# Performance work log

Measured on AMD Instinct MI355X. Metric: run time of the kernel, lower is better.

The kernel has to match this reference:

```python
import jax, jax.numpy as jnp
import numpy as np

H, D = 16, 64          # num_heads, head_dim
OUT = H * D            # out_dim = 1024
W1, W2 = 32, 32        # sliding windows
EPS_NORM = 1e-7
EPS_LN = 1e-5


def setup_inputs() -> dict:
    key = jax.random.key(0)
    ks = jax.random.split(key, 6)
    B, S, IN = 2, 2048, 1024
    x = jax.random.normal(ks[0], (B, S, IN), dtype=jnp.float32)
    scale = 0.02
    W_Q = jax.random.normal(ks[1], (IN, OUT), dtype=jnp.float32) * scale
    W_K = jax.random.normal(ks[2], (IN, OUT), dtype=jnp.float32) * scale
    W_V = jax.random.normal(ks[3], (IN, OUT), dtype=jnp.float32) * scale
    W_Kp = jax.random.normal(ks[4], (IN, OUT), dtype=jnp.float32) * scale
    W_O = jax.random.normal(ks[5], (OUT, OUT), dtype=jnp.float32) * scale
    ln_gamma = jnp.ones((OUT,), dtype=jnp.float32)
    ln_beta = jnp.zeros((OUT,), dtype=jnp.float32)
    return {"x": x, "W_Q": W_Q, "W_K": W_K, "W_V": W_V, "W_Kp": W_Kp,
            "W_O": W_O, "ln_gamma": ln_gamma, "ln_beta": ln_beta}


def _l2norm(t):
    return t / (jnp.linalg.norm(t, axis=-1, keepdims=True) + EPS_NORM)


def reference(x, W_Q, W_K, W_V, W_Kp, W_O, ln_gamma, ln_beta):
    B, S, _ = x.shape
    # projections -> (B, S, H, D)
    Q = _l2norm((x @ W_Q).reshape(B, S, H, D))
    K = _l2norm((x @ W_K).reshape(B, S, H, D))
    Kp = _l2norm((x @ W_Kp).reshape(B, S, H, D))
    V = (x @ W_V).reshape(B, S, H, D)
    # windowed keys/values (last w1/w2 positions, as in the PyTorch fallback)
    K_win = K[:, -W1:]
    Kp_win = Kp[:, -W2:]
    V_win = V[:, -W1:]
    Vp_win = V[:, -W2:]
    # triple product A_ijk = q.k.k' / sqrt(D) -> (B, S, H, w1, w2)
    A = jnp.einsum('bshd,bjhd,bkhd->bshjk', Q, K_win, Kp_win) / jnp.sqrt(jnp.float32(D))
    # causal window mask: allow j <= i + w1 - S and k <= i + w2 - S
    s_idx = jnp.arange(S)[:, None, None]
    j_idx = jnp.arange(W1)[None, :, None]
    k_idx = jnp.arange(W2)[None, None, :]
    mask = (j_idx > s_idx + (W1 - S)) | (k_idx > s_idx + (W2 - S))  # (S, w1, w2)
    neg_inf = jnp.float32(-jnp.inf)
    A = jnp.where(mask[None, :, None, :, :], neg_inf, A)
    # joint softmax over (j, k); fully-masked query rows produce zeros
    A_flat = A.reshape(B, S, H, W1 * W2)
    all_masked = jnp.all(A_flat == neg_inf, axis=-1, keepdims=True)
    A_safe = jnp.where(all_masked, 0.0, A_flat)
    P = jax.nn.softmax(A_safe, axis=-1)
    P = jnp.where(all_masked, 0.0, P).reshape(B, S, H, W1, W2)
    # value outer-product weighting (V' = V)
    Z = jnp.einsum('bshjk,bjhd,bkhd->bshd', P, V_win, Vp_win)
    out = Z.reshape(B, S, OUT) @ W_O
    out = out + x  # residual (shapes match)
    # LayerNorm
    mu = jnp.mean(out, axis=-1, keepdims=True)
    var = jnp.mean((out - mu) ** 2, axis=-1, keepdims=True)
    out = (out - mu) / jnp.sqrt(var + EPS_LN) * ln_gamma + ln_beta
    return out
```

## Files before the change

kernel.cpp:

```cpp
#include <hip/hip_runtime.h>
#include <math.h>


#define XS 68

#define YP_STR   262144
#define NKS_P    8
#define ZF_OFF   (NKS_P * YP_STR)
#define DP_OFF   (ZF_OFF + 65536)
#define DP_STR   65536
#define NKS_W    16

__global__ __launch_bounds__(256, 4) void proj_kernel(
    const float* __restrict__ x,
    const float* __restrict__ Wq, const float* __restrict__ Wk,
    const float* __restrict__ Wkp, const float* __restrict__ Wv,
    float* __restrict__ Y) {
  __shared__ float xs[64 * 65];
  __shared__ float wl[64 * 68];
  const int tid  = threadIdx.x;
  const int cb   = blockIdx.x;
  const int ks   = blockIdx.y;
  const int col0 = cb * 64;
  const int z    = cb >> 4;
  const int colz = col0 & 1023;
  const float* __restrict__ W =
      (z == 0) ? Wq : ((z == 1) ? Wk : ((z == 2) ? Wkp : Wv));

  const int wave = __builtin_amdgcn_readfirstlane(tid >> 6);
  const int lane = tid & 63;

  float acc[16];
  #pragma unroll
  for (int c = 0; c < 16; c++) acc[c] = 0.f;

  for (int cc = 0; cc < 2; cc++) {
    const int kb = ks * 128 + cc * 64;
    #pragma unroll
    for (int i = 0; i < 4; i++) {
      int e = i * 256 + tid;
      int r = e >> 4, q = e & 15;
      int b = r >> 5, t = r & 31;
      float4 v = *(const float4*)(x + ((b * 2048 + 2016 + t) * 1024 + kb + q * 4));
      xs[(q * 4 + 0) * 65 + r] = v.x;
      xs[(q * 4 + 1) * 65 + r] = v.y;
      xs[(q * 4 + 2) * 65 + r] = v.z;
      xs[(q * 4 + 3) * 65 + r] = v.w;
    }
    #pragma unroll
    for (int i = 0; i < 4; i++) {
      int e = i * 256 + tid;
      int r = e >> 4, q = e & 15;
      float4 v = *(const float4*)(W + (size_t)(kb + r) * 1024 + colz + q * 4);
      float* d = wl + r * 68 + q * 4;
      d[0] = v.x; d[1] = v.y; d[2] = v.z; d[3] = v.w;
    }
    __syncthreads();

    const float* __restrict__ wbase = wl + wave * 16;
    #pragma unroll 4
    for (int kk = 0; kk < 64; kk++) {
      float xv = xs[kk * 65 + lane];
      const float* __restrict__ wrow = wbase + kk * 68;
      #pragma unroll
      for (int c = 0; c < 16; c++) acc[c] = fmaf(xv, wrow[c], acc[c]);
    }
    __syncthreads();
  }

  #pragma unroll
  for (int c = 0; c < 16; c++) xs[lane * 65 + wave * 16 + c] = acc[c];
  __syncthreads();
  float* __restrict__ Yo = Y + ks * YP_STR + col0;
  #pragma unroll
  for (int i = 0; i < 16; i++) {
    int r = wave * 16 + i;
    Yo[r * 4096 + lane] = xs[r * 65 + lane];
  }
}

__global__ __launch_bounds__(256) void attn_kernel(
    const float* __restrict__ Y, float* __restrict__ Zout) {
  __shared__ float Kn[32 * XS], Kp[32 * XS], Vs[32 * XS];
  __shared__ float Pt[4][32 * 33];
  __shared__ float qs[4][64];
  const int tid = threadIdx.x;
  const int wave = tid >> 6, lane = tid & 63;
  const int h = blockIdx.y, b = blockIdx.z;

  #pragma unroll
  for (int i = 0; i < 8; i++) {
    int e = i * 256 + tid;
    int row = e >> 6, d = e & 63;
    int src = (b * 32 + row) * 4096 + h * 64 + d;
    float kn = 0.f, kp = 0.f, vv = 0.f;
    #pragma unroll
    for (int p = 0; p < NKS_P; p++) {
      const float* Yp = Y + p * YP_STR + src;
      kn += Yp[1024]; kp += Yp[2048]; vv += Yp[3072];
    }
    Kn[row * XS + d] = kn; Kp[row * XS + d] = kp; Vs[row * XS + d] = vv;
  }
  __syncthreads();

  for (int rr = 0; rr < 8; rr++) {
    int row = wave * 8 + rr;
    float kv = Kn[row * XS + lane];
    float s2 = kv * kv;
    #pragma unroll
    for (int off = 1; off < 64; off <<= 1) s2 += __shfl_xor(s2, off);
    Kn[row * XS + lane] = kv * (1.f / (sqrtf(s2) + 1e-7f));
    float pv = Kp[row * XS + lane];
    float p2 = pv * pv;
    #pragma unroll
    for (int off = 1; off < 64; off <<= 1) p2 += __shfl_xor(p2, off);
    Kp[row * XS + lane] = pv * (1.f / (sqrtf(p2) + 1e-7f));
  }
  __syncthreads();

  const int m = blockIdx.x * 4 + wave;
  const int r = b * 32 + m;

  float q = 0.f;
  #pragma unroll
  for (int p = 0; p < NKS_P; p++) q += Y[p * YP_STR + r * 4096 + h * 64 + lane];
  float q2 = q * q;
  #pragma unroll
  for (int off = 1; off < 64; off <<= 1) q2 += __shfl_xor(q2, off);
  q *= (1.f / (sqrtf(q2) + 1e-7f));
  qs[wave][lane] = q;
  __builtin_amdgcn_wave_barrier();

  const int lj = lane >> 3, lk = lane & 7;
  float acc[4][4];
  #pragma unroll
  for (int a = 0; a < 4; a++)
    #pragma unroll
    for (int c = 0; c < 4; c++) acc[a][c] = 0.f;

  const float* qw = qs[wave];
  for (int dq = 0; dq < 16; dq++) {
    float4 q4 = *(const float4*)(qw + dq * 4);
    float4 t4[4], kp4[4];
    #pragma unroll
    for (int tj = 0; tj < 4; tj++) {
      float4 kv = *(const float4*)(Kn + (lj * 4 + tj) * XS + dq * 4);
      t4[tj].x = q4.x * kv.x; t4[tj].y = q4.y * kv.y;
      t4[tj].z = q4.z * kv.z; t4[tj].w = q4.w * kv.w;
    }
    #pragma unroll
    for (int tk = 0; tk < 4; tk++)
      kp4[tk] = *(const float4*)(Kp + (lk * 4 + tk) * XS + dq * 4);
    #pragma unroll
    for (int tj = 0; tj < 4; tj++)
      #pragma unroll
      for (int tk = 0; tk < 4; tk++)
        acc[tj][tk] += t4[tj].x * kp4[tk].x + t4[tj].y * kp4[tk].y
                     + t4[tj].z * kp4[tk].z + t4[tj].w * kp4[tk].w;
  }

  float amax = -1e30f;
  #pragma unroll
  for (int tj = 0; tj < 4; tj++)
    #pragma unroll
    for (int tk = 0; tk < 4; tk++) {
      int j = lj * 4 + tj, k = lk * 4 + tk;
      if (j <= m && k <= m) amax = fmaxf(amax, acc[tj][tk] * 0.125f);
    }
  #pragma unroll
  for (int off = 1; off < 64; off <<= 1) amax = fmaxf(amax, __shfl_xor(amax, off));

  float lsum = 0.f;
  float* ptw = Pt[wave];
  #pragma unroll
  for (int tj = 0; tj < 4; tj++)
    #pragma unroll
    for (int tk = 0; tk < 4; tk++) {
      int j = lj * 4 + tj, k = lk * 4 + tk;
      float e = 0.f;
      if (j <= m && k <= m) e = __expf(acc[tj][tk] * 0.125f - amax);
      lsum += e;
      ptw[k * 33 + j] = e;
    }
  #pragma unroll
  for (int off = 1; off < 64; off <<= 1) lsum += __shfl_xor(lsum, off);
  float inv = 1.f / lsum;
  __builtin_amdgcn_wave_barrier();

  float vreg[32];
  #pragma unroll
  for (int k = 0; k < 32; k++) vreg[k] = Vs[k * XS + lane];
  float zacc = 0.f;
  for (int k = 0; k <= m; k++) {
    float g = 0.f;
    #pragma unroll
    for (int j = 0; j < 32; j++) g += ptw[k * 33 + j] * vreg[j];
    zacc += g * vreg[k];
  }
  Zout[r * 1024 + h * 64 + lane] = zacc * inv;
}

__global__ __launch_bounds__(256, 4) void wo_kernel(
    const float* __restrict__ Zr, const float* __restrict__ Wo,
    float* __restrict__ Dp) {
  __shared__ float xs[64 * 65];
  __shared__ float wl[64 * 68];
  const int tid  = threadIdx.x;
  const int col0 = blockIdx.x * 64;
  const int ks   = blockIdx.y;
  const int kb   = ks * 64;

  const int wave = __builtin_amdgcn_readfirstlane(tid >> 6);
  const int lane = tid & 63;

  #pragma unroll
  for (int i = 0; i < 4; i++) {
    int e = i * 256 + tid;
    int r = e >> 4, q = e & 15;
    float4 v = *(const float4*)(Zr + r * 1024 + kb + q * 4);
    xs[(q * 4 + 0) * 65 + r] = v.x;
    xs[(q * 4 + 1) * 65 + r] = v.y;
    xs[(q * 4 + 2) * 65 + r] = v.z;
    xs[(q * 4 + 3) * 65 + r] = v.w;
  }
  #pragma unroll
  for (int i = 0; i < 4; i++) {
    int e = i * 256 + tid;
    int r = e >> 4, q = e & 15;
    float4 v = *(const float4*)(Wo + (size_t)(kb + r) * 1024 + col0 + q * 4);
    float* d = wl + r * 68 + q * 4;
    d[0] = v.x; d[1] = v.y; d[2] = v.z; d[3] = v.w;
  }
  __syncthreads();

  float acc[16];
  #pragma unroll
  for (int c = 0; c < 16; c++) acc[c] = 0.f;

  const float* __restrict__ wbase = wl + wave * 16;
  #pragma unroll 4
  for (int kk = 0; kk < 64; kk++) {
    float xv = xs[kk * 65 + lane];
    const float* __restrict__ wrow = wbase + kk * 68;
    #pragma unroll
    for (int c = 0; c < 16; c++) acc[c] = fmaf(xv, wrow[c], acc[c]);
  }

  __syncthreads();
  #pragma unroll
  for (int c = 0; c < 16; c++) xs[lane * 65 + wave * 16 + c] = acc[c];
  __syncthreads();
  float* __restrict__ D = Dp + ks * DP_STR + col0;
  #pragma unroll
  for (int i = 0; i < 16; i++) {
    int r = wave * 16 + i;
    D[r * 1024 + lane] = xs[r * 65 + lane];
  }
}

__global__ __launch_bounds__(256, 4) void ln_kernel(
    const float4* __restrict__ x4, const float4* __restrict__ dp4,
    const float4* __restrict__ g4, const float4* __restrict__ b4,
    float4* __restrict__ out4) {
  const int tid = threadIdx.x;
  const int wave = tid >> 6, lane = tid & 63;
  const int row = blockIdx.x * 4 + wave;
  const int b = row >> 11, s = row & 2047;

  float4 v[4];
  #pragma unroll
  for (int i = 0; i < 4; i++) v[i] = x4[row * 256 + i * 64 + lane];
  if (s >= 2016) {
    int drow = b * 32 + (s - 2016);
    #pragma unroll
    for (int p = 0; p < NKS_W; p++) {
      #pragma unroll
      for (int i = 0; i < 4; i++) {
        float4 d = dp4[p * 16384 + drow * 256 + i * 64 + lane];
        v[i].x += d.x; v[i].y += d.y; v[i].z += d.z; v[i].w += d.w;
      }
    }
  }
  float sum = 0.f, ss = 0.f;
  #pragma unroll
  for (int i = 0; i < 4; i++) {
    sum += v[i].x + v[i].y + v[i].z + v[i].w;
    ss  += v[i].x * v[i].x + v[i].y * v[i].y + v[i].z * v[i].z + v[i].w * v[i].w;
  }
  #pragma unroll
  for (int off = 1; off < 64; off <<= 1) {
    sum += __shfl_xor(sum, off);
    ss  += __shfl_xor(ss, off);
  }
  float mu   = sum * (1.f / 1024.f);
  float var  = ss * (1.f / 1024.f) - mu * mu;
  float rstd = rsqrtf(var + 1e-5f);

  #pragma unroll
  for (int i = 0; i < 4; i++) {
    float4 g = g4[i * 64 + lane];
    float4 be = b4[i * 64 + lane];
    float4 o;
    o.x = (v[i].x - mu) * rstd * g.x + be.x;
    o.y = (v[i].y - mu) * rstd * g.y + be.y;
    o.z = (v[i].z - mu) * rstd * g.z + be.z;
    o.w = (v[i].w - mu) * rstd * g.w + be.w;
    out4[row * 256 + i * 64 + lane] = o;
  }
}

extern "C" void kernel_launch(void* const* d_in, const int* in_sizes, int n_in,
                              void* d_out, int out_size, void* d_ws, size_t ws_size,
                              hipStream_t stream) {
  const float* x   = (const float*)d_in[0];
  const float* Wq  = (const float*)d_in[1];
  const float* Wk  = (const float*)d_in[2];
  const float* Wv  = (const float*)d_in[3];
  const float* Wkp = (const float*)d_in[4];
  const float* Wo  = (const float*)d_in[5];
  const float* gam = (const float*)d_in[6];
  const float* bet = (const float*)d_in[7];
  float* out = (float*)d_out;
  float* ws  = (float*)d_ws;

  hipLaunchKernelGGL(proj_kernel, dim3(64, NKS_P), dim3(256), 0, stream,
                     x, Wq, Wk, Wkp, Wv, ws);
  hipLaunchKernelGGL(attn_kernel, dim3(8, 16, 2), dim3(256), 0, stream,
                     ws, ws + ZF_OFF);
  hipLaunchKernelGGL(wo_kernel, dim3(16, NKS_W), dim3(256), 0, stream,
                     ws + ZF_OFF, Wo, ws + DP_OFF);
  hipLaunchKernelGGL(ln_kernel, dim3(1024), dim3(256), 0, stream,
                     (const float4*)x, (const float4*)(ws + DP_OFF),
                     (const float4*)gam, (const float4*)bet, (float4*)out);
}
```

Before: 136.4 us.

## Fuse non-window LayerNorm into projection launch and use 4x4 register tiles

Query rows outside the last 32 positions get zero attention output, so their LayerNorm needs only x. That work now runs in extra blocks of the projection launch, overlapping the projection GEMM, and the final LN kernel handles only the 64 window rows. The projection and W_O GEMM tiles switch from one-column-per-lane with 16 accumulators to 4x4 register micro-tiles with float4 shared-memory loads and direct float4 stores, removing the shared-memory transpose epilogue. The cost is a mixed-role kernel whose LN blocks may compete with the GEMM blocks for CU slots.

```diff
diff --git a/kernel.cpp b/kernel.cpp
--- a/kernel.cpp
+++ b/kernel.cpp
@@ -3,6 +3,7 @@
 
 
 #define XS 68
+#define WS 68
 
 #define YP_STR   262144
 #define NKS_P    8
@@ -11,71 +12,124 @@
 #define DP_STR   65536
 #define NKS_W    16
 
-__global__ __launch_bounds__(256, 4) void proj_kernel(
+__device__ __forceinline__ void ln_row(
+    const float4* __restrict__ x4, const float4* __restrict__ g4,
+    const float4* __restrict__ b4, float4* __restrict__ out4,
+    int row, int lane) {
+  float4 v[4];
+  #pragma unroll
+  for (int i = 0; i < 4; i++) v[i] = x4[row * 256 + i * 64 + lane];
+  float sum = 0.f, ss = 0.f;
+  #pragma unroll
+  for (int i = 0; i < 4; i++) {
+    sum += v[i].x + v[i].y + v[i].z + v[i].w;
+    ss  += v[i].x * v[i].x + v[i].y * v[i].y + v[i].z * v[i].z + v[i].w * v[i].w;
+  }
+  #pragma unroll
+  for (int off = 1; off < 64; off <<= 1) {
+    sum += __shfl_xor(sum, off);
+    ss  += __shfl_xor(ss, off);
+  }
+  float mu   = sum * (1.f / 1024.f);
+  float rstd = rsqrtf(ss * (1.f / 1024.f) - mu * mu + 1e-5f);
+  #pragma unroll
+  for (int i = 0; i < 4; i++) {
+    float4 g  = g4[i * 64 + lane];
+    float4 be = b4[i * 64 + lane];
+    float4 o;
+    o.x = (v[i].x - mu) * rstd * g.x + be.x;
+    o.y = (v[i].y - mu) * rstd * g.y + be.y;
+    o.z = (v[i].z - mu) * rstd * g.z + be.z;
+    o.w = (v[i].w - mu) * rstd * g.w + be.w;
+    out4[row * 256 + i * 64 + lane] = o;
+  }
+}
+
+__global__ __launch_bounds__(256, 4) void proj_ln_kernel(
     const float* __restrict__ x,
     const float* __restrict__ Wq, const float* __restrict__ Wk,
     const float* __restrict__ Wkp, const float* __restrict__ Wv,
-    float* __restrict__ Y) {
-  __shared__ float xs[64 * 65];
-  __shared__ float wl[64 * 68];
-  const int tid  = threadIdx.x;
-  const int cb   = blockIdx.x;
-  const int ks   = blockIdx.y;
-  const int col0 = cb * 64;
-  const int z    = cb >> 4;
-  const int colz = col0 & 1023;
-  const float* __restrict__ W =
-      (z == 0) ? Wq : ((z == 1) ? Wk : ((z == 2) ? Wkp : Wv));
-
-  const int wave = __builtin_amdgcn_readfirstlane(tid >> 6);
-  const int lane = tid & 63;
-
-  float acc[16];
-  #pragma unroll
-  for (int c = 0; c < 16; c++) acc[c] = 0.f;
-
-  for (int cc = 0; cc < 2; cc++) {
-    const int kb = ks * 128 + cc * 64;
+    const float* __restrict__ gam, const float* __restrict__ bet,
+    float* __restrict__ Y, float* __restrict__ out) {
+  __shared__ float xs[64 * WS];
+  __shared__ float wl[64 * WS];
+  const int tid = threadIdx.x;
+  const int bid = blockIdx.x;
+
+  if (bid < 512) {
+    const int cb   = bid & 63;
+    const int ks   = bid >> 6;
+    const int col0 = cb * 64;
+    const int z    = cb >> 4;
+    const int colz = col0 & 1023;
+    const float* __restrict__ W =
+        (z == 0) ? Wq : ((z == 1) ? Wk : ((z == 2) ? Wkp : Wv));
+    const int tc = tid & 15, tr = tid >> 4;
+
+    float acc[4][4];
+    #pragma unroll
+    for (int i = 0; i < 4; i++)
+      #pragma unroll
+      for (int j = 0; j < 4; j++) acc[i][j] = 0.f;
+
+    for (int cc = 0; cc < 2; cc++) {
+      const int kb = ks * 128 + cc * 64;
+      #pragma unroll
+      for (int i = 0; i < 4; i++) {
+        int e = i * 256 + tid;
+        int r = e >> 4, q = e & 15;
+        int b = r >> 5, t = r & 31;
+        float4 v = *(const float4*)(x + ((b * 2048 + 2016 + t) * 1024 + kb + q * 4));
+        xs[(q * 4 + 0) * WS + r] = v.x;
+        xs[(q * 4 + 1) * WS + r] = v.y;
+        xs[(q * 4 + 2) * WS + r] = v.z;
+        xs[(q * 4 + 3) * WS + r] = v.w;
+        float4 w = *(const float4*)(W + (size_t)(kb + r) * 1024 + colz + q * 4);
+        *(float4*)(wl + r * WS + q * 4) = w;
+      }
+      __syncthreads();
+
+      #pragma unroll 8
+      for (int kk = 0; kk < 64; kk++) {
+        float4 xv = *(const float4*)(xs + kk * WS + tr * 4);
+        float4 wv = *(const float4*)(wl + kk * WS + tc * 4);
+        acc[0][0] = fmaf(xv.x, wv.x, acc[0][0]);
+        acc[0][1] = fmaf(xv.x, wv.y, acc[0][1]);
+        acc[0][2] = fmaf(xv.x, wv.z, acc[0][2]);
+        acc[0][3] = fmaf(xv.x, wv.w, acc[0][3]);
+        acc[1][0] = fmaf(xv.y, wv.x, acc[1][0]);
+        acc[1][1] = fmaf(xv.y, wv.y, acc[1][1]);
+        acc[1][2] = fmaf(xv.y, wv.z, acc[1][2]);
+        acc[1][3] = fmaf(xv.y, wv.w, acc[1][3]);
+        acc[2][0] = fmaf(xv.z, wv.x, acc[2][0]);
+        acc[2][1] = fmaf(xv.z, wv.y, acc[2][1]);
+        acc[2][2] = fmaf(xv.z, wv.z, acc[2][2]);
+        acc[2][3] = fmaf(xv.z, wv.w, acc[2][3]);
+        acc[3][0] = fmaf(xv.w, wv.x, acc[3][0]);
+        acc[3][1] = fmaf(xv.w, wv.y, acc[3][1]);
+        acc[3][2] = fmaf(xv.w, wv.z, acc[3][2]);
+        acc[3][3] = fmaf(xv.w, wv.w, acc[3][3]);
+      }
+      __syncthreads();
+    }
+
+    float* __restrict__ Yo = Y + ks * YP_STR + col0;
     #pragma unroll
     for (int i = 0; i < 4; i++) {
-      int e = i * 256 + tid;
-      int r = e >> 4, q = e & 15;
-      int b = r >> 5, t = r & 31;
-      float4 v = *(const float4*)(x + ((b * 2048 + 2016 + t) * 1024 + kb + q * 4));
-      xs[(q * 4 + 0) * 65 + r] = v.x;
-      xs[(q * 4 + 1) * 65 + r] = v.y;
-      xs[(q * 4 + 2) * 65 + r] = v.z;
-      xs[(q * 4 + 3) * 65 + r] = v.w;
-    }
-    #pragma unroll
-    for (int i = 0; i < 4; i++) {
-      int e = i * 256 + tid;
-      int r = e >> 4, q = e & 15;
-      float4 v = *(const float4*)(W + (size_t)(kb + r) * 1024 + colz + q * 4);
-      float* d = wl + r * 68 + q * 4;
-      d[0] = v.x; d[1] = v.y; d[2] = v.z; d[3] = v.w;
-    }
-    __syncthreads();
-
-    const float* __restrict__ wbase = wl + wave * 16;
-    #pragma unroll 4
-    for (int kk = 0; kk < 64; kk++) {
-      float xv = xs[kk * 65 + lane];
-      const float* __restrict__ wrow = wbase + kk * 68;
-      #pragma unroll
-      for (int c = 0; c < 16; c++) acc[c] = fmaf(xv, wrow[c], acc[c]);
-    }
-    __syncthreads();
-  }
-
-  #pragma unroll
-  for (int c = 0; c < 16; c++) xs[lane * 65 + wave * 16 + c] = acc[c];
-  __syncthreads();
-  float* __restrict__ Yo = Y + ks * YP_STR + col0;
-  #pragma unroll
-  for (int i = 0; i < 16; i++) {
-    int r = wave * 16 + i;
-    Yo[r * 4096 + lane] = xs[r * 65 + lane];
+      float4 o = make_float4(acc[i][0], acc[i][1], acc[i][2], acc[i][3]);
+      *(float4*)(Yo + (tr * 4 + i) * 4096 + tc * 4) = o;
+    }
+  } else {
+    const int wave = tid >> 6, lane = tid & 63;
+    const int gw = (bid - 512) * 4 + wave;
+    const float4* x4 = (const float4*)x;
+    const float4* g4 = (const float4*)gam;
+    const float4* b4 = (const float4*)bet;
+    float4* out4 = (float4*)out;
+    for (int idx = gw; idx < 4032; idx += 1792) {
+      int row = (idx < 2016) ? idx : idx + 32;
+      ln_row(x4, g4, b4, out4, row, lane);
+    }
   }
 }
 
@@ -203,82 +257,82 @@
 __global__ __launch_bounds__(256, 4) void wo_kernel(
     const float* __restrict__ Zr, const float* __restrict__ Wo,
     float* __restrict__ Dp) {
-  __shared__ float xs[64 * 65];
-  __shared__ float wl[64 * 68];
+  __shared__ float zs[64 * WS];
+  __shared__ float wl[64 * WS];
   const int tid  = threadIdx.x;
   const int col0 = blockIdx.x * 64;
   const int ks   = blockIdx.y;
   const int kb   = ks * 64;
-
-  const int wave = __builtin_amdgcn_readfirstlane(tid >> 6);
-  const int lane = tid & 63;
+  const int tc = tid & 15, tr = tid >> 4;
 
   #pragma unroll
   for (int i = 0; i < 4; i++) {
     int e = i * 256 + tid;
     int r = e >> 4, q = e & 15;
     float4 v = *(const float4*)(Zr + r * 1024 + kb + q * 4);
-    xs[(q * 4 + 0) * 65 + r] = v.x;
-    xs[(q * 4 + 1) * 65 + r] = v.y;
-    xs[(q * 4 + 2) * 65 + r] = v.z;
-    xs[(q * 4 + 3) * 65 + r] = v.w;
-  }
-  #pragma unroll
-  for (int i = 0; i < 4; i++) {
-    int e = i * 256 + tid;
-    int r = e >> 4, q = e & 15;
-    float4 v = *(const float4*)(Wo + (size_t)(kb + r) * 1024 + col0 + q * 4);
-    float* d = wl + r * 68 + q * 4;
-    d[0] = v.x; d[1] = v.y; d[2] = v.z; d[3] = v.w;
+    zs[(q * 4 + 0) * WS + r] = v.x;
+    zs[(q * 4 + 1) * WS + r] = v.y;
+    zs[(q * 4 + 2) * WS + r] = v.z;
+    zs[(q * 4 + 3) * WS + r] = v.w;
+    float4 w = *(const float4*)(Wo + (size_t)(kb + r) * 1024 + col0 + q * 4);
+    *(float4*)(wl + r * WS + q * 4) = w;
   }
   __syncthreads();
 
-  float acc[16];
-  #pragma unroll
-  for (int c = 0; c < 16; c++) acc[c] = 0.f;
-
-  const float* __restrict__ wbase = wl + wave * 16;
-  #pragma unroll 4
+  float acc[4][4];
+  #pragma unroll
+  for (int i = 0; i < 4; i++)
+    #pragma unroll
+    for (int j = 0; j < 4; j++) acc[i][j] = 0.f;
+
+  #pragma unroll 8
   for (int kk = 0; kk < 64; kk++) {
-    float xv = xs[kk * 65 + lane];
-    const float* __restrict__ wrow = wbase + kk * 68;
-    #pragma unroll
-    for (int c = 0; c < 16; c++) acc[c] = fmaf(xv, wrow[c], acc[c]);
-  }
-
-  __syncthreads();
-  #pragma unroll
-  for (int c = 0; c < 16; c++) xs[lane * 65 + wave * 16 + c] = acc[c];
-  __syncthreads();
+    float4 xv = *(const float4*)(zs + kk * WS + tr * 4);
+    float4 wv = *(const float4*)(wl + kk * WS + tc * 4);
+    acc[0][0] = fmaf(xv.x, wv.x, acc[0][0]);
+    acc[0][1] = fmaf(xv.x, wv.y, acc[0][1]);
+    acc[0][2] = fmaf(xv.x, wv.z, acc[0][2]);
+    acc[0][3] = fmaf(xv.x, wv.w, acc[0][3]);
+    acc[1][0] = fmaf(xv.y, wv.x, acc[1][0]);
+    acc[1][1] = fmaf(xv.y, wv.y, acc[1][1]);
+    acc[1][2] = fmaf(xv.y, wv.z, acc[1][2]);
+    acc[1][3] = fmaf(xv.y, wv.w, acc[1][3]);
+    acc[2][0] = fmaf(xv.z, wv.x, acc[2][0]);
+    acc[2][1] = fmaf(xv.z, wv.y, acc[2][1]);
+    acc[2][2] = fmaf(xv.z, wv.z, acc[2][2]);
+    acc[2][3] = fmaf(xv.z, wv.w, acc[2][3]);
+    acc[3][0] = fmaf(xv.w, wv.x, acc[3][0]);
+    acc[3][1] = fmaf(xv.w, wv.y, acc[3][1]);
+    acc[3][2] = fmaf(xv.w, wv.z, acc[3][2]);
+    acc[3][3] = fmaf(xv.w, wv.w, acc[3][3]);
+  }
+
   float* __restrict__ D = Dp + ks * DP_STR + col0;
   #pragma unroll
-  for (int i = 0; i < 16; i++) {
-    int r = wave * 16 + i;
-    D[r * 1024 + lane] = xs[r * 65 + lane];
-  }
-}
-
-__global__ __launch_bounds__(256, 4) void ln_kernel(
+  for (int i = 0; i < 4; i++) {
+    float4 o = make_float4(acc[i][0], acc[i][1], acc[i][2], acc[i][3]);
+    *(float4*)(D + (tr * 4 + i) * 1024 + tc * 4) = o;
+  }
+}
+
+__global__ __launch_bounds__(256, 4) void ln_win_kernel(
     const float4* __restrict__ x4, const float4* __restrict__ dp4,
     const float4* __restrict__ g4, const float4* __restrict__ b4,
     float4* __restrict__ out4) {
   const int tid = threadIdx.x;
   const int wave = tid >> 6, lane = tid & 63;
-  const int row = blockIdx.x * 4 + wave;
-  const int b = row >> 11, s = row & 2047;
+  const int wr  = blockIdx.x * 4 + wave;
+  const int row = (wr >> 5) * 2048 + 2016 + (wr & 31);
 
   float4 v[4];
   #pragma unroll
   for (int i = 0; i < 4; i++) v[i] = x4[row * 256 + i * 64 + lane];
-  if (s >= 2016) {
-    int drow = b * 32 + (s - 2016);
-    #pragma unroll
-    for (int p = 0; p < NKS_W; p++) {
-      #pragma unroll
-      for (int i = 0; i < 4; i++) {
-        float4 d = dp4[p * 16384 + drow * 256 + i * 64 + lane];
-        v[i].x += d.x; v[i].y += d.y; v[i].z += d.z; v[i].w += d.w;
-      }
+  #pragma unroll
+  for (int p = 0; p < NKS_W; p++) {
+    #pragma unroll
+    for (int i = 0; i < 4; i++) {
+      float4 d = dp4[p * 16384 + wr * 256 + i * 64 + lane];
+      v[i].x += d.x; v[i].y += d.y; v[i].z += d.z; v[i].w += d.w;
     }
   }
   float sum = 0.f, ss = 0.f;
@@ -293,8 +347,7 @@
     ss  += __shfl_xor(ss, off);
   }
   float mu   = sum * (1.f / 1024.f);
-  float var  = ss * (1.f / 1024.f) - mu * mu;
-  float rstd = rsqrtf(var + 1e-5f);
+  float rstd = rsqrtf(ss * (1.f / 1024.f) - mu * mu + 1e-5f);
 
   #pragma unroll
   for (int i = 0; i < 4; i++) {
@@ -323,13 +376,13 @@
   float* out = (float*)d_out;
   float* ws  = (float*)d_ws;
 
-  hipLaunchKernelGGL(proj_kernel, dim3(64, NKS_P), dim3(256), 0, stream,
-                     x, Wq, Wk, Wkp, Wv, ws);
+  hipLaunchKernelGGL(proj_ln_kernel, dim3(512 + 448), dim3(256), 0, stream,
+                     x, Wq, Wk, Wkp, Wv, gam, bet, ws, out);
   hipLaunchKernelGGL(attn_kernel, dim3(8, 16, 2), dim3(256), 0, stream,
                      ws, ws + ZF_OFF);
   hipLaunchKernelGGL(wo_kernel, dim3(16, NKS_W), dim3(256), 0, stream,
                      ws + ZF_OFF, Wo, ws + DP_OFF);
-  hipLaunchKernelGGL(ln_kernel, dim3(1024), dim3(256), 0, stream,
+  hipLaunchKernelGGL(ln_win_kernel, dim3(16), dim3(256), 0, stream,
                      (const float4*)x, (const float4*)(ws + DP_OFF),
                      (const float4*)gam, (const float4*)bet, (float4*)out);
 }
```

Result: faster. 128.8 us (-5.6%).
